# Kernel optimization log

Hardware: AMD Instinct MI355X
Metric: run time of the kernel (lower is better)

The kernel has to match this reference:

```python
import jax, jax.numpy as jnp
import numpy as np

IN_FEATURES = 1024
OUT_FEATURES = 1024
GRID_SIZE = 5
SPLINE_ORDER = 3
N_BASIS = GRID_SIZE + SPLINE_ORDER  # 8, matches spline_weight last dim
N_GRID = GRID_SIZE + 2 * SPLINE_ORDER + 1  # 12 knots -> Cox-de-Boor yields N_BASIS bases


def b_spline(x, grid):
    # x: [B, I] -> bases: [B, I, N_BASIS]
    x = x[..., None]
    bases = ((x >= grid[:-1]) & (x < grid[1:])).astype(x.dtype)
    for k in range(1, SPLINE_ORDER + 1):
        left = (x - grid[: -k - 1]) / (grid[k:-1] - grid[: -k - 1] + 1e-8)
        right = (grid[k + 1:] - x) / (grid[k + 1:] - grid[1:-k] + 1e-8)
        bases = left * bases[..., :-1] + right * bases[..., 1:]
    return bases


def setup_inputs() -> dict:
    key = jax.random.key(0)
    k1, k2, k3 = jax.random.split(key, 3)
    x = jax.random.uniform(k1, (4096, IN_FEATURES), dtype=jnp.float32) * 2.0 - 1.0
    # kaiming_uniform_(a=sqrt(5)) on [out,in]: bound = 1/sqrt(in)
    bound = 1.0 / np.sqrt(IN_FEATURES)
    base_weight = jax.random.uniform(k2, (OUT_FEATURES, IN_FEATURES), dtype=jnp.float32,
                                     minval=-bound, maxval=bound)
    spline_weight = 0.1 * jax.random.normal(k3, (OUT_FEATURES, IN_FEATURES, N_BASIS), dtype=jnp.float32)
    grid = jnp.linspace(-1.0, 1.0, N_GRID, dtype=jnp.float32)
    return {"x": x, "base_weight": base_weight, "spline_weight": spline_weight, "grid": grid}


def reference(x, base_weight, spline_weight, grid):
    base_output = jax.nn.silu(x) @ base_weight.T  # [B, O]
    spline_basis = b_spline(x, grid)              # [B, I, Q]
    spline_output = jnp.einsum('biq,oiq->bo', spline_basis, spline_weight)
    return base_output + spline_output
```

## Files before the change

### kernel.cpp

```cpp
#include <hip/hip_runtime.h>
#include <hip/hip_bf16.h>

#define IN_F 1024
#define OUT_F 1024
#define QP 9
#define KDIM (IN_F * QP)
#define SPLITK 2
#define KSLICE (KDIM / SPLITK)
#define BK 64

typedef __attribute__((ext_vector_type(8)))  short short8;
typedef __attribute__((ext_vector_type(16))) float floatx16;
typedef __attribute__((ext_vector_type(8)))  unsigned short ushort8v;

__device__ __forceinline__ unsigned short f2bf(float f) {
    union { float f; unsigned u; } v; v.f = f;
    return (unsigned short)((v.u + 0x7FFF + ((v.u >> 16) & 1)) >> 16);
}

__global__ __launch_bounds__(256) void pack_kernel(const float* __restrict__ x,
                                                   const float* __restrict__ bw,
                                                   const float* __restrict__ sw,
                                                   __hip_bfloat16* __restrict__ A,
                                                   __hip_bfloat16* __restrict__ W, int Bm) {
    const int nb_a = (Bm * IN_F / 8) / 256;
    if ((int)blockIdx.x < nb_a) {
        int t  = blockIdx.x * 256 + threadIdx.x;
        int b  = t >> 7;
        int i0 = (t & 127) * 8;
        const float4* xr = (const float4*)(x + (size_t)b * IN_F + i0);
        float4 x0 = xr[0], x1 = xr[1];
        float xv[8] = {x0.x, x0.y, x0.z, x0.w, x1.x, x1.y, x1.z, x1.w};
        ushort8v ov[9];
#pragma unroll
        for (int e = 0; e < 8; ++e) {
            float v  = xv[e];
            float u  = (v + 1.0f) * 5.5f;
            float fj = floorf(u);
            int   j  = (int)fj;
            float tt = u - fj;
            float t2 = tt * tt, t3 = t2 * tt;
            float omt = 1.0f - tt;
            float w0 = omt * omt * omt * (1.0f / 6.0f);
            float w1 = (3.0f * t3 - 6.0f * t2 + 4.0f) * (1.0f / 6.0f);
            float w2 = (-3.0f * t3 + 3.0f * t2 + 3.0f * tt + 1.0f) * (1.0f/6.0f);
            float w3 = t3 * (1.0f / 6.0f);
            ov[0][e] = f2bf(v * __builtin_amdgcn_rcpf(1.0f + __expf(-v)));
#pragma unroll
            for (int q = 0; q < 8; ++q) {
                int d = j - q;
                float bv = (d == 3) ? w0 : (d == 2) ? w1 : (d == 1) ? w2 : (d == 0) ? w3 : 0.0f;
                ov[1 + q][e] = f2bf(bv);
            }
        }
        unsigned short* dst = (unsigned short*)A + (size_t)b * KDIM + i0;
#pragma unroll
        for (int s = 0; s < QP; ++s)
            *(ushort8v*)(dst + (size_t)s * IN_F) = ov[s];
    } else {
        int t = ((int)blockIdx.x - nb_a) * 256 + threadIdx.x;
        unsigned short* dst = (unsigned short*)W + (size_t)(t >> 10) * KDIM + (t & 1023);
        dst[0] = f2bf(bw[t]);
        const float4* s4 = (const float4*)(sw + (size_t)t * 8);
        float4 lo = s4[0], hi = s4[1];
        dst[1 * IN_F] = f2bf(lo.x); dst[2 * IN_F] = f2bf(lo.y);
        dst[3 * IN_F] = f2bf(lo.z); dst[4 * IN_F] = f2bf(lo.w);
        dst[5 * IN_F] = f2bf(hi.x); dst[6 * IN_F] = f2bf(hi.y);
        dst[7 * IN_F] = f2bf(hi.z); dst[8 * IN_F] = f2bf(hi.w);
    }
}

__global__ __launch_bounds__(256, 2) void gemm_splitk(const __hip_bfloat16* __restrict__ A,
                                                      const __hip_bfloat16* __restrict__ W,
                                                      float* __restrict__ P, int Bm) {
    __shared__ short sA[128 * BK];
    __shared__ short sB[128 * BK];
    const int tid   = threadIdx.x;
    const int lane  = tid & 63;
    const int wave  = tid >> 6;
    const int row32 = lane & 31;
    const int half  = lane >> 5;
    const int wm = wave >> 1, wn = wave & 1;
    const int m0 = blockIdx.y * 128;
    const int n0 = blockIdx.x * 128;
    const int kb = blockIdx.z * KSLICE;

    const short* Ag = (const short*)A + (size_t)m0 * KDIM + kb;
    const short* Wg = (const short*)W + (size_t)n0 * KDIM + kb;

    floatx16 acc[2][2] = {};

    int rs[4], ko[4], ld[4];
#pragma unroll
    for (int p = 0; p < 4; ++p) {
        int c = p * 256 + tid;
        rs[p] = c >> 3;
        ko[p] = (((c & 7) ^ ((rs[p] >> 1) & 7)) * 8);
        ld[p] = c * 8;
    }

    const int rA0 = wm * 64 + row32,      rA1 = rA0 + 32;
    const int rB0 = wn * 64 + row32,      rB1 = rB0 + 32;
    const int swA0 = (rA0 >> 1) & 7, swA1 = (rA1 >> 1) & 7;
    const int swB0 = (rB0 >> 1) & 7, swB1 = (rB1 >> 1) & 7;

    for (int k0 = 0; k0 < KSLICE; k0 += BK) {
#pragma unroll
        for (int p = 0; p < 4; ++p)
            __builtin_amdgcn_global_load_lds(
                (const __attribute__((address_space(1))) void*)(Ag + (size_t)rs[p] * KDIM + k0 + ko[p]),
                (__attribute__((address_space(3))) void*)(sA + ld[p]), 16, 0, 0);
#pragma unroll
        for (int p = 0; p < 4; ++p)
            __builtin_amdgcn_global_load_lds(
                (const __attribute__((address_space(1))) void*)(Wg + (size_t)rs[p] * KDIM + k0 + ko[p]),
                (__attribute__((address_space(3))) void*)(sB + ld[p]), 16, 0, 0);
        __syncthreads();

#pragma unroll
        for (int ks = 0; ks < 4; ++ks) {
            int c = ks * 2 + half;
            short8 aF[2], bF[2];
            aF[0] = *(const short8*)&sA[rA0 * BK + ((c ^ swA0) * 8)];
            aF[1] = *(const short8*)&sA[rA1 * BK + ((c ^ swA1) * 8)];
            bF[0] = *(const short8*)&sB[rB0 * BK + ((c ^ swB0) * 8)];
            bF[1] = *(const short8*)&sB[rB1 * BK + ((c ^ swB1) * 8)];
#pragma unroll
            for (int mi = 0; mi < 2; ++mi)
#pragma unroll
                for (int ni = 0; ni < 2; ++ni)
                    acc[mi][ni] = __builtin_amdgcn_mfma_f32_32x32x16_bf16(
                        aF[mi], bF[ni], acc[mi][ni], 0, 0, 0);
        }
        __syncthreads();
    }

    float* Pz = P + (size_t)blockIdx.z * Bm * OUT_F;
#pragma unroll
    for (int mi = 0; mi < 2; ++mi)
#pragma unroll
        for (int ni = 0; ni < 2; ++ni)
#pragma unroll
            for (int r = 0; r < 16; ++r) {
                int row = (r & 3) + 8 * (r >> 2) + 4 * half;
                int gm  = m0 + wm * 64 + mi * 32 + row;
                Pz[(size_t)gm * OUT_F + n0 + wn * 64 + ni * 32 + row32] = acc[mi][ni][r];
            }
}

__global__ __launch_bounds__(256) void reduce_kernel(const float4* __restrict__ P,
                                                     float4* __restrict__ C, int n4) {
    int t = blockIdx.x * 256 + threadIdx.x;
    float4 a = P[t], b = P[n4 + t];
    float4 o;
    o.x = a.x + b.x; o.y = a.y + b.y; o.z = a.z + b.z; o.w = a.w + b.w;
    C[t] = o;
}

__global__ __launch_bounds__(256) void fallback_kernel(const float* __restrict__ x,
                                                       const float* __restrict__ bw,
                                                       const float* __restrict__ sw,
                                                       const float* __restrict__ grid,
                                                       float* __restrict__ out, int Bm) {
    __shared__ float sv[256][QP + 1];
    int b = blockIdx.y;
    int o = blockIdx.x * 256 + threadIdx.x;
    float acc = 0.f;
    for (int ic = 0; ic < IN_F; ic += 256) {
        int i = ic + threadIdx.x;
        float v = x[(size_t)b * IN_F + i];
        float g[12];
        for (int j = 0; j < 12; ++j) g[j] = grid[j];
        float bb[11];
        for (int j = 0; j < 11; ++j) bb[j] = (v >= g[j] && v < g[j + 1]) ? 1.f : 0.f;
        for (int k = 1; k <= 3; ++k)
            for (int j = 0; j < 11 - k; ++j)
                bb[j] = (v - g[j]) / (g[j + k] - g[j] + 1e-8f) * bb[j]
                      + (g[j + k + 1] - v) / (g[j + k + 1] - g[j + 1] + 1e-8f) * bb[j + 1];
        __syncthreads();
        sv[threadIdx.x][0] = v / (1.f + __expf(-v));
        for (int q = 0; q < 8; ++q) sv[threadIdx.x][1 + q] = bb[q];
        __syncthreads();
        for (int ii = 0; ii < 256; ++ii) {
            int i2 = ic + ii;
            acc += sv[ii][0] * bw[(size_t)o * IN_F + i2];
            const float* swp = sw + ((size_t)o * IN_F + i2) * 8;
            for (int q = 0; q < 8; ++q) acc += sv[ii][1 + q] * swp[q];
        }
    }
    out[(size_t)b * OUT_F + o] = acc;
}

extern "C" void kernel_launch(void* const* d_in, const int* in_sizes, int n_in,
                              void* d_out, int out_size, void* d_ws, size_t ws_size,
                              hipStream_t stream) {
    const float* x    = (const float*)d_in[0];
    const float* bw   = (const float*)d_in[1];
    const float* sw   = (const float*)d_in[2];
    const float* grid = (const float*)d_in[3];
    float* out = (float*)d_out;

    const int Bm = in_sizes[0] / IN_F;
    const size_t a_bytes = (size_t)Bm * KDIM * sizeof(__hip_bfloat16);
    const size_t w_bytes = (size_t)OUT_F * KDIM * sizeof(__hip_bfloat16);
    const size_t p_bytes = (size_t)SPLITK * Bm * OUT_F * sizeof(float);

    if (ws_size >= a_bytes + w_bytes && (Bm % 128) == 0) {
        __hip_bfloat16* Apk = (__hip_bfloat16*)d_ws;
        __hip_bfloat16* Wpk = (__hip_bfloat16*)((char*)d_ws + a_bytes);
        const int nb_a = (Bm * IN_F / 8) / 256;
        const int nb_w = (OUT_F * IN_F) / 256;
        pack_kernel<<<nb_a + nb_w, 256, 0, stream>>>(x, bw, sw, Apk, Wpk, Bm);
        if (ws_size >= a_bytes + w_bytes + p_bytes) {
            float* P = (float*)((char*)d_ws + a_bytes + w_bytes);
            gemm_splitk<<<dim3(OUT_F / 128, Bm / 128, SPLITK), 256, 0, stream>>>(Apk, Wpk, P, Bm);
            reduce_kernel<<<Bm * OUT_F / 1024, 256, 0, stream>>>((const float4*)P, (float4*)out,
                                                                 Bm * OUT_F / 4);
        } else {
            gemm_splitk<<<dim3(OUT_F / 128, Bm / 128, 1), 256, 0, stream>>>(Apk, Wpk, out, Bm);
        }
    } else {
        fallback_kernel<<<dim3(OUT_F / 256, Bm), 256, 0, stream>>>(x, bw, sw, grid, out, Bm);
    }
}
```

Before: 216.8 us.

## Register-prefetch global loads, raise split-K to three, adjust occupancy

```diff
diff --git a/kernel.cpp b/kernel.cpp
--- a/kernel.cpp
+++ b/kernel.cpp
@@ -5,7 +5,7 @@
 #define OUT_F 1024
 #define QP 9
 #define KDIM (IN_F * QP)
-#define SPLITK 2
+#define SPLITK 3
 #define KSLICE (KDIM / SPLITK)
 #define BK 64
 
@@ -70,7 +70,7 @@
     }
 }
 
-__global__ __launch_bounds__(256, 2) void gemm_splitk(const __hip_bfloat16* __restrict__ A,
+__global__ __launch_bounds__(256, 3) void gemm_splitk(const __hip_bfloat16* __restrict__ A,
                                                       const __hip_bfloat16* __restrict__ W,
                                                       float* __restrict__ P, int Bm) {
     __shared__ short sA[128 * BK];
@@ -99,23 +99,34 @@
         ld[p] = c * 8;
     }
 
-    const int rA0 = wm * 64 + row32,      rA1 = rA0 + 32;
-    const int rB0 = wn * 64 + row32,      rB1 = rB0 + 32;
+    const int rA0 = wm * 64 + row32, rA1 = rA0 + 32;
+    const int rB0 = wn * 64 + row32, rB1 = rB0 + 32;
     const int swA0 = (rA0 >> 1) & 7, swA1 = (rA1 >> 1) & 7;
     const int swB0 = (rB0 >> 1) & 7, swB1 = (rB1 >> 1) & 7;
 
+    uint4 gA[4], gB[4];
+#pragma unroll
+    for (int p = 0; p < 4; ++p) {
+        gA[p] = *(const uint4*)(Ag + (size_t)rs[p] * KDIM + ko[p]);
+        gB[p] = *(const uint4*)(Wg + (size_t)rs[p] * KDIM + ko[p]);
+    }
+
     for (int k0 = 0; k0 < KSLICE; k0 += BK) {
-#pragma unroll
-        for (int p = 0; p < 4; ++p)
-            __builtin_amdgcn_global_load_lds(
-                (const __attribute__((address_space(1))) void*)(Ag + (size_t)rs[p] * KDIM + k0 + ko[p]),
-                (__attribute__((address_space(3))) void*)(sA + ld[p]), 16, 0, 0);
-#pragma unroll
-        for (int p = 0; p < 4; ++p)
-            __builtin_amdgcn_global_load_lds(
-                (const __attribute__((address_space(1))) void*)(Wg + (size_t)rs[p] * KDIM + k0 + ko[p]),
-                (__attribute__((address_space(3))) void*)(sB + ld[p]), 16, 0, 0);
-        __syncthreads();
+        __syncthreads();
+#pragma unroll
+        for (int p = 0; p < 4; ++p) {
+            *(uint4*)(sA + ld[p]) = gA[p];
+            *(uint4*)(sB + ld[p]) = gB[p];
+        }
+        __syncthreads();
+
+        if (k0 + BK < KSLICE) {
+#pragma unroll
+            for (int p = 0; p < 4; ++p) {
+                gA[p] = *(const uint4*)(Ag + (size_t)rs[p] * KDIM + k0 + BK + ko[p]);
+                gB[p] = *(const uint4*)(Wg + (size_t)rs[p] * KDIM + k0 + BK + ko[p]);
+            }
+        }
 
 #pragma unroll
         for (int ks = 0; ks < 4; ++ks) {
@@ -132,7 +143,6 @@
                     acc[mi][ni] = __builtin_amdgcn_mfma_f32_32x32x16_bf16(
                         aF[mi], bF[ni], acc[mi][ni], 0, 0, 0);
         }
-        __syncthreads();
     }
 
     float* Pz = P + (size_t)blockIdx.z * Bm * OUT_F;
@@ -151,9 +161,12 @@
 __global__ __launch_bounds__(256) void reduce_kernel(const float4* __restrict__ P,
                                                      float4* __restrict__ C, int n4) {
     int t = blockIdx.x * 256 + threadIdx.x;
-    float4 a = P[t], b = P[n4 + t];
+    float4 a = P[t], b = P[n4 + t], c = P[2 * n4 + t];
     float4 o;
-    o.x = a.x + b.x; o.y = a.y + b.y; o.z = a.z + b.z; o.w = a.w + b.w;
+    o.x = a.x + b.x + c.x;
+    o.y = a.y + b.y + c.y;
+    o.z = a.z + b.z + c.z;
+    o.w = a.w + b.w + c.w;
     C[t] = o;
 }
 
@@ -205,20 +218,16 @@
     const size_t w_bytes = (size_t)OUT_F * KDIM * sizeof(__hip_bfloat16);
     const size_t p_bytes = (size_t)SPLITK * Bm * OUT_F * sizeof(float);
 
-    if (ws_size >= a_bytes + w_bytes && (Bm % 128) == 0) {
+    if (ws_size >= a_bytes + w_bytes + p_bytes && (Bm % 128) == 0) {
         __hip_bfloat16* Apk = (__hip_bfloat16*)d_ws;
         __hip_bfloat16* Wpk = (__hip_bfloat16*)((char*)d_ws + a_bytes);
+        float* P = (float*)((char*)d_ws + a_bytes + w_bytes);
         const int nb_a = (Bm * IN_F / 8) / 256;
         const int nb_w = (OUT_F * IN_F) / 256;
         pack_kernel<<<nb_a + nb_w, 256, 0, stream>>>(x, bw, sw, Apk, Wpk, Bm);
-        if (ws_size >= a_bytes + w_bytes + p_bytes) {
-            float* P = (float*)((char*)d_ws + a_bytes + w_bytes);
-            gemm_splitk<<<dim3(OUT_F / 128, Bm / 128, SPLITK), 256, 0, stream>>>(Apk, Wpk, P, Bm);
-            reduce_kernel<<<Bm * OUT_F / 1024, 256, 0, stream>>>((const float4*)P, (float4*)out,
-                                                                 Bm * OUT_F / 4);
-        } else {
-            gemm_splitk<<<dim3(OUT_F / 128, Bm / 128, 1), 256, 0, stream>>>(Apk, Wpk, out, Bm);
-        }
+        gemm_splitk<<<dim3(OUT_F / 128, Bm / 128, SPLITK), 256, 0, stream>>>(Apk, Wpk, P, Bm);
+        reduce_kernel<<<Bm * OUT_F / 1024, 256, 0, stream>>>((const float4*)P, (float4*)out,
+                                                             Bm * OUT_F / 4);
     } else {
         fallback_kernel<<<dim3(OUT_F / 256, Bm), 256, 0, stream>>>(x, bw, sw, grid, out, Bm);
     }
```

Result: slower. 495.2 us (+128.5%).
